# Optimization experiments

Hardware: AMD Instinct MI355X
Metric: run time of the kernel (lower is better)

Reference implementation:

```python
import jax, jax.numpy as jnp
import numpy as np

K_CHAINS, N_STATES, ALPHABET, SEQ_LEN = 3, 12, 32, 64


def setup_inputs() -> dict:
    key = jax.random.key(0)
    k0, k1, k2, k3, k4 = jax.random.split(key, 5)
    return {
        "ys": jax.random.randint(k0, (SEQ_LEN,), 0, ALPHABET),
        "transition": jax.random.normal(k1, (K_CHAINS, N_STATES, N_STATES), jnp.float32),
        "emission": jax.random.normal(k2, (K_CHAINS, N_STATES, ALPHABET), jnp.float32),
        "choice": jax.random.normal(k3, (K_CHAINS,), jnp.float32),
        "prior": jax.random.normal(k4, (K_CHAINS, N_STATES), jnp.float32),
    }


def reference(ys, transition, emission, choice, prior):
    K, S = transition.shape[0], transition.shape[1]
    c = jax.nn.log_softmax(choice)                  # (K,)
    t = jax.nn.log_softmax(transition, axis=-1)     # (K,S,S)
    e = jax.nn.log_softmax(emission, axis=-1)       # (K,S,A)
    p = jax.nn.log_softmax(prior, axis=-1)          # (K,S)

    # enumerate expanded state space: tuples (s_1..s_K, i) -> N = S^K * K rows
    grids = jnp.meshgrid(*([jnp.arange(S)] * K + [jnp.arange(K)]), indexing="ij")
    tbl = jnp.stack(grids, -1).reshape(-1, K + 1)   # (N, K+1)
    states = tbl[:, :K]                             # (N, K) chain states
    chain = tbl[:, K]                               # (N,)   active chain index

    # transition matrix A[m, n] = logprob(old expanded state n -> new expanded state m)
    onehot = jax.nn.one_hot(chain, K, dtype=bool)   # (N, K)
    eq = states[:, None, :] == states[None, :, :]   # (N_new, N_old, K)
    valid = jnp.where(onehot[:, None, :], True, eq).all(-1)  # non-active chains unchanged
    s_new = jnp.take_along_axis(states, chain[:, None], axis=1)[:, 0]  # (N,) new state of active chain
    s_old = states[:, chain]                        # (N_old, N_new): old state at chain[m]
    t_term = t[chain[None, :], s_old, s_new[None, :]]  # (N_old, N_new)
    Amat = c[chain][:, None] + t_term.T + jnp.where(valid, 0.0, -jnp.inf)  # (N_new, N_old)

    # emission table B[m, y] = e[chain[m], state of active chain, y]
    B = e[chain, s_new]                             # (N, A)

    # initial alpha: sum_j p[j, s_j] + c[i]
    alpha0 = p[jnp.arange(K)[None, :], states].sum(-1) + c[chain]  # (N,)

    def step(alpha, y):
        alpha = B[:, y] + jax.nn.logsumexp(alpha[None, :] + Amat, axis=-1)
        return alpha, None

    alpha, _ = jax.lax.scan(step, alpha0, ys)
    return jax.nn.logsumexp(alpha)
```

## Files before the change

kernel.cpp:

```cpp
#include <hip/hip_runtime.h>
#include <math.h>

#define KC 3
#define S 12
#define SS 1728
#define AB 32
#define TLEN 64
#define NTHREADS 448
#define NWAVES 7
#define NSLICE 432
#define ROWW 13
#define LN2F 0.69314718055994530942f

__global__ __launch_bounds__(NTHREADS, 2)
void hmm_fwd_kernel(const int* __restrict__ ys,
                    const float* __restrict__ transition,
                    const float* __restrict__ emission,
                    const float* __restrict__ choice,
                    const float* __restrict__ prior,
                    float* __restrict__ out)
{
    __shared__ float P0[144*ROWW], P1[144*ROWW], P2[144*ROWW];
    __shared__ float BR[144*ROWW], BQ[144*ROWW], BP[144*ROWW];
    __shared__ float ECt[KC*AB*S];
    __shared__ float T_s[KC][S][S];
    __shared__ float p_lin[KC][S];
    __shared__ float c_lin[KC];
    __shared__ int   ys_s[TLEN];
    __shared__ float wsum[NWAVES];

    const int tid = threadIdx.x;

    if (tid < TLEN) ys_s[tid] = ys[tid];

    if (tid == 0) {
        float m = fmaxf(fmaxf(choice[0], choice[1]), choice[2]);
        float e0 = __expf(choice[0]-m), e1 = __expf(choice[1]-m), e2 = __expf(choice[2]-m);
        float inv = 1.f / (e0+e1+e2);
        c_lin[0] = e0*inv; c_lin[1] = e1*inv; c_lin[2] = e2*inv;
    }
    if (tid >= 1 && tid < 1 + KC) {
        int k = tid - 1;
        float m = -INFINITY;
        #pragma unroll
        for (int i = 0; i < S; ++i) m = fmaxf(m, prior[k*S + i]);
        float ev[S]; float s = 0.f;
        #pragma unroll
        for (int i = 0; i < S; ++i) { ev[i] = __expf(prior[k*S + i] - m); s += ev[i]; }
        float inv = 1.f / s;
        #pragma unroll
        for (int i = 0; i < S; ++i) p_lin[k][i] = ev[i] * inv;
    }
    if (tid >= 64 && tid < 64 + KC*S) {
        int r = tid - 64;
        int k = r / S, i = r % S;
        const float* row = transition + (k*S + i)*S;
        float m = -INFINITY;
        #pragma unroll
        for (int j = 0; j < S; ++j) m = fmaxf(m, row[j]);
        float ev[S]; float s = 0.f;
        #pragma unroll
        for (int j = 0; j < S; ++j) { ev[j] = __expf(row[j] - m); s += ev[j]; }
        float inv = 1.f / s;
        #pragma unroll
        for (int j = 0; j < S; ++j) T_s[k][i][j] = ev[j] * inv;
    }
    if (tid >= 128 && tid < 128 + KC*S) {
        int r = tid - 128;
        int k = r / S, sj = r % S;
        float cm = fmaxf(fmaxf(choice[0], choice[1]), choice[2]);
        float ce = __expf(choice[k]-cm) /
                   (__expf(choice[0]-cm) + __expf(choice[1]-cm) + __expf(choice[2]-cm));
        const float* row = emission + (k*S + sj)*AB;
        float m = -INFINITY;
        #pragma unroll
        for (int a = 0; a < AB; ++a) m = fmaxf(m, row[a]);
        float ev[AB]; float s = 0.f;
        #pragma unroll
        for (int a = 0; a < AB; ++a) { ev[a] = __expf(row[a] - m); s += ev[a]; }
        float inv = ce / s;
        #pragma unroll
        for (int a = 0; a < AB; ++a) ECt[(k*AB + a)*S + sj] = ev[a] * inv;
    }
    __syncthreads();

    const bool active = tid < NSLICE;
    const int sk = tid / 144;
    const int q  = tid % 144;

    const float* rdp = (sk == 0) ? &BR[ROWW*q] : (sk == 1) ? &BQ[ROWW*q] : &BP[ROWW*q];
    float*       wrp = (sk == 0) ? &P0[ROWW*q] : (sk == 1) ? &P1[ROWW*q] : &P2[ROWW*q];
    const float* ecb = &ECt[sk*AB*S];

    const int s0f = tid / 36;
    const int s1f = (4*tid % 144) / 12;
    const int s2b = (4*tid) % 12;
    const int bRo = ROWW*(12*s1f + s2b) + s0f;
    const int bQo = ROWW*(12*s0f + s2b) + s1f;
    const int bPo = ROWW*(12*s0f + s1f) + s2b;

    float Treg[S][S];
    if (active) {
        #pragma unroll
        for (int i = 0; i < S; ++i) {
            #pragma unroll
            for (int j = 0; j < S; ++j) {
                float tmp = T_s[sk][i][j];
                asm volatile("v_mov_b32 %0, %1" : "=v"(Treg[i][j]) : "v"(tmp));
            }
        }
        float pq = (sk == 0) ? p_lin[1][q/12] * p_lin[2][q%12]
                 : (sk == 1) ? p_lin[0][q/12] * p_lin[2][q%12]
                 :             p_lin[0][q/12] * p_lin[1][q%12];
        float ck = c_lin[sk];
        #pragma unroll
        for (int j = 0; j < S; ++j) wrp[j] = p_lin[sk][j] * pq * ck;
    }
    __syncthreads();

    float logR = 0.f, invR = 1.f;

    for (int t = 0; t < TLEN; ++t) {
        const int y = ys_s[t];

        if (active) {
            float b[4];
            #pragma unroll
            for (int e = 0; e < 4; ++e) {
                float r = P0[bRo + ROWW*e];
                float g = P1[bQo + ROWW*e];
                float h = P2[bPo + e];
                b[e] = (r + g + h) * invR;
            }
            #pragma unroll
            for (int e = 0; e < 4; ++e) {
                BR[bRo + ROWW*e] = b[e];
                BQ[bQo + ROWW*e] = b[e];
                BP[bPo + e]      = b[e];
            }
        }
        __syncthreads();

        float o[S];
        if (active) {
            const float* eb = &ecb[y*S];
            float4 e0 = *reinterpret_cast<const float4*>(&eb[0]);
            float4 e1 = *reinterpret_cast<const float4*>(&eb[4]);
            float4 e2 = *reinterpret_cast<const float4*>(&eb[8]);

            float bv[S];
            #pragma unroll
            for (int i = 0; i < S; ++i) bv[i] = rdp[i];

            float acc[S];
            #pragma unroll
            for (int j = 0; j < S; ++j) acc[j] = 0.f;
            #pragma unroll
            for (int i = 0; i < S; ++i) {
                const float bb = bv[i];
                #pragma unroll
                for (int j = 0; j < S; ++j) acc[j] = __builtin_fmaf(bb, Treg[i][j], acc[j]);
            }
            o[0] = acc[0]*e0.x; o[1] = acc[1]*e0.y; o[2]  = acc[2]*e0.z;  o[3]  = acc[3]*e0.w;
            o[4] = acc[4]*e1.x; o[5] = acc[5]*e1.y; o[6]  = acc[6]*e1.z;  o[7]  = acc[7]*e1.w;
            o[8] = acc[8]*e2.x; o[9] = acc[9]*e2.y; o[10] = acc[10]*e2.z; o[11] = acc[11]*e2.w;

            #pragma unroll
            for (int j = 0; j < S; ++j) wrp[j] = o[j];
        }

        if ((t & 7) == 7) {
            float part = 0.f;
            if (active) {
                #pragma unroll
                for (int j = 0; j < S; ++j) part += o[j];
            }
            #pragma unroll
            for (int w = 32; w > 0; w >>= 1) part += __shfl_xor(part, w);
            if ((tid & 63) == 0) wsum[tid >> 6] = part;
        }
        __syncthreads();

        if ((t & 7) == 7 && t < TLEN-1) {
            float R = wsum[0];
            #pragma unroll
            for (int w = 1; w < NWAVES; ++w) R += wsum[w];
            invR = __builtin_amdgcn_rcpf(R);
            logR += __log2f(R);
        } else {
            invR = 1.f;
        }
    }

    if (tid == 0) {
        float R = wsum[0];
        #pragma unroll
        for (int w = 1; w < NWAVES; ++w) R += wsum[w];
        out[0] = LN2F * (__log2f(R) + logR);
    }
}

extern "C" void kernel_launch(void* const* d_in, const int* in_sizes, int n_in,
                              void* d_out, int out_size, void* d_ws, size_t ws_size,
                              hipStream_t stream) {
    const int*   ys         = (const int*)  d_in[0];
    const float* transition = (const float*)d_in[1];
    const float* emission   = (const float*)d_in[2];
    const float* choice     = (const float*)d_in[3];
    const float* prior      = (const float*)d_in[4];
    float* out = (float*)d_out;

    hipLaunchKernelGGL(hmm_fwd_kernel, dim3(1), dim3(NTHREADS), 0, stream,
                       ys, transition, emission, choice, prior, out);
}
```

Baseline: 71.25 us.

## Fuse gather-sum into step with double-buffered planes, one barrier per step

Drops the separate gather/scatter phase (BR/BQ/BP buffers) and its extra barrier. Each thread now reads the two foreign-chain planes directly with strided LDS loads and keeps its own slice in registers. The per-step output is double-buffered so only one __syncthreads is needed per time step. Transition rows are no longer pinned in registers but read from LDS as float4 broadcasts each step, which trades register pressure for extra LDS traffic.

```diff
diff --git a/kernel.cpp b/kernel.cpp
--- a/kernel.cpp
+++ b/kernel.cpp
@@ -9,7 +9,6 @@
 #define NTHREADS 448
 #define NWAVES 7
 #define NSLICE 432
-#define ROWW 13
 #define LN2F 0.69314718055994530942f
 
 __global__ __launch_bounds__(NTHREADS, 2)
@@ -20,10 +19,9 @@
                     const float* __restrict__ prior,
                     float* __restrict__ out)
 {
-    __shared__ float P0[144*ROWW], P1[144*ROWW], P2[144*ROWW];
-    __shared__ float BR[144*ROWW], BQ[144*ROWW], BP[144*ROWW];
-    __shared__ float ECt[KC*AB*S];
-    __shared__ float T_s[KC][S][S];
+    __shared__ __align__(16) float PL[2][KC][SS];
+    __shared__ __align__(16) float T_s[KC][S][S];
+    __shared__ __align__(16) float ECt[KC][AB][S];
     __shared__ float p_lin[KC][S];
     __shared__ float c_lin[KC];
     __shared__ int   ys_s[TLEN];
@@ -80,100 +78,112 @@
         for (int a = 0; a < AB; ++a) { ev[a] = __expf(row[a] - m); s += ev[a]; }
         float inv = ce / s;
         #pragma unroll
-        for (int a = 0; a < AB; ++a) ECt[(k*AB + a)*S + sj] = ev[a] * inv;
+        for (int a = 0; a < AB; ++a) ECt[k][a][sj] = ev[a] * inv;
     }
     __syncthreads();
 
     const bool active = tid < NSLICE;
-    const int sk = tid / 144;
-    const int q  = tid % 144;
-
-    const float* rdp = (sk == 0) ? &BR[ROWW*q] : (sk == 1) ? &BQ[ROWW*q] : &BP[ROWW*q];
-    float*       wrp = (sk == 0) ? &P0[ROWW*q] : (sk == 1) ? &P1[ROWW*q] : &P2[ROWW*q];
-    const float* ecb = &ECt[sk*AB*S];
-
-    const int s0f = tid / 36;
-    const int s1f = (4*tid % 144) / 12;
-    const int s2b = (4*tid) % 12;
-    const int bRo = ROWW*(12*s1f + s2b) + s0f;
-    const int bQo = ROWW*(12*s0f + s2b) + s1f;
-    const int bPo = ROWW*(12*s0f + s1f) + s2b;
-
-    float Treg[S][S];
+    const int ct = active ? tid : (NSLICE - 1);
+    const int sk = ct / 144;
+    const int q  = ct % 144;
+    const int qh = q / 12, ql = q % 12;
+
+    int offA, offB;
+    if (sk == 0)      { offA = 12*ql + qh;        offB = 12*qh + ql;        }
+    else if (sk == 1) { offA = 12*ql + qh;        offB = 144*qh + ql;       }
+    else              { offA = 144*ql + qh;       offB = 144*qh + ql;       }
+
+    const int fApl = (sk == 0) ? 1 : 0;
+    const int fBpl = (sk == 2) ? 1 : 2;
+
+    const float* Tp  = &T_s[sk][0][0];
+    const float* ecp = &ECt[sk][0][0];
+
+    const float* fA0 = &PL[0][fApl][offA];
+    const float* fB0 = &PL[0][fBpl][offB];
+    float*       wp0 = &PL[0][sk][12*q];
+    const float* fA1 = &PL[1][fApl][offA];
+    const float* fB1 = &PL[1][fBpl][offB];
+    float*       wp1 = &PL[1][sk][12*q];
+
+    float own[S];
     if (active) {
-        #pragma unroll
-        for (int i = 0; i < S; ++i) {
-            #pragma unroll
-            for (int j = 0; j < S; ++j) {
-                float tmp = T_s[sk][i][j];
-                asm volatile("v_mov_b32 %0, %1" : "=v"(Treg[i][j]) : "v"(tmp));
-            }
-        }
-        float pq = (sk == 0) ? p_lin[1][q/12] * p_lin[2][q%12]
-                 : (sk == 1) ? p_lin[0][q/12] * p_lin[2][q%12]
-                 :             p_lin[0][q/12] * p_lin[1][q%12];
+        float pq = (sk == 0) ? p_lin[1][qh] * p_lin[2][ql]
+                 : (sk == 1) ? p_lin[0][qh] * p_lin[2][ql]
+                 :             p_lin[0][qh] * p_lin[1][ql];
         float ck = c_lin[sk];
         #pragma unroll
-        for (int j = 0; j < S; ++j) wrp[j] = p_lin[sk][j] * pq * ck;
+        for (int j = 0; j < S; ++j) {
+            own[j] = p_lin[sk][j] * pq * ck;
+            wp0[j] = own[j];
+        }
     }
     __syncthreads();
 
     float logR = 0.f, invR = 1.f;
 
-    for (int t = 0; t < TLEN; ++t) {
+    auto do_step = [&](int t, const float* fA, const float* fB, float* wp) {
         const int y = ys_s[t];
-
         if (active) {
-            float b[4];
-            #pragma unroll
-            for (int e = 0; e < 4; ++e) {
-                float r = P0[bRo + ROWW*e];
-                float g = P1[bQo + ROWW*e];
-                float h = P2[bPo + e];
-                b[e] = (r + g + h) * invR;
-            }
-            #pragma unroll
-            for (int e = 0; e < 4; ++e) {
-                BR[bRo + ROWW*e] = b[e];
-                BQ[bQo + ROWW*e] = b[e];
-                BP[bPo + e]      = b[e];
-            }
-        }
-        __syncthreads();
-
-        float o[S];
-        if (active) {
-            const float* eb = &ecb[y*S];
+            const float* eb = ecp + y*S;
             float4 e0 = *reinterpret_cast<const float4*>(&eb[0]);
             float4 e1 = *reinterpret_cast<const float4*>(&eb[4]);
             float4 e2 = *reinterpret_cast<const float4*>(&eb[8]);
 
+            float fa[S], fb[S];
+            if (sk == 0) {
+                #pragma unroll
+                for (int i = 0; i < S; ++i) { fa[i] = fA[144*i]; fb[i] = fB[144*i]; }
+            } else if (sk == 1) {
+                #pragma unroll
+                for (int i = 0; i < S; ++i) { fa[i] = fA[144*i]; fb[i] = fB[12*i]; }
+            } else {
+                #pragma unroll
+                for (int i = 0; i < S; ++i) { fa[i] = fA[12*i];  fb[i] = fB[12*i]; }
+            }
+
             float bv[S];
             #pragma unroll
-            for (int i = 0; i < S; ++i) bv[i] = rdp[i];
+            for (int i = 0; i < S; ++i) bv[i] = (own[i] + fa[i] + fb[i]) * invR;
 
             float acc[S];
             #pragma unroll
             for (int j = 0; j < S; ++j) acc[j] = 0.f;
             #pragma unroll
             for (int i = 0; i < S; ++i) {
+                float4 t0 = *reinterpret_cast<const float4*>(&Tp[12*i + 0]);
+                float4 t1 = *reinterpret_cast<const float4*>(&Tp[12*i + 4]);
+                float4 t2 = *reinterpret_cast<const float4*>(&Tp[12*i + 8]);
                 const float bb = bv[i];
-                #pragma unroll
-                for (int j = 0; j < S; ++j) acc[j] = __builtin_fmaf(bb, Treg[i][j], acc[j]);
+                acc[0] = __builtin_fmaf(bb, t0.x, acc[0]);
+                acc[1] = __builtin_fmaf(bb, t0.y, acc[1]);
+                acc[2] = __builtin_fmaf(bb, t0.z, acc[2]);
+                acc[3] = __builtin_fmaf(bb, t0.w, acc[3]);
+                acc[4] = __builtin_fmaf(bb, t1.x, acc[4]);
+                acc[5] = __builtin_fmaf(bb, t1.y, acc[5]);
+                acc[6] = __builtin_fmaf(bb, t1.z, acc[6]);
+                acc[7] = __builtin_fmaf(bb, t1.w, acc[7]);
+                acc[8] = __builtin_fmaf(bb, t2.x, acc[8]);
+                acc[9] = __builtin_fmaf(bb, t2.y, acc[9]);
+                acc[10] = __builtin_fmaf(bb, t2.z, acc[10]);
+                acc[11] = __builtin_fmaf(bb, t2.w, acc[11]);
             }
-            o[0] = acc[0]*e0.x; o[1] = acc[1]*e0.y; o[2]  = acc[2]*e0.z;  o[3]  = acc[3]*e0.w;
-            o[4] = acc[4]*e1.x; o[5] = acc[5]*e1.y; o[6]  = acc[6]*e1.z;  o[7]  = acc[7]*e1.w;
-            o[8] = acc[8]*e2.x; o[9] = acc[9]*e2.y; o[10] = acc[10]*e2.z; o[11] = acc[11]*e2.w;
-
-            #pragma unroll
-            for (int j = 0; j < S; ++j) wrp[j] = o[j];
+
+            own[0]=acc[0]*e0.x; own[1]=acc[1]*e0.y; own[2] =acc[2]*e0.z;  own[3] =acc[3]*e0.w;
+            own[4]=acc[4]*e1.x; own[5]=acc[5]*e1.y; own[6] =acc[6]*e1.z;  own[7] =acc[7]*e1.w;
+            own[8]=acc[8]*e2.x; own[9]=acc[9]*e2.y; own[10]=acc[10]*e2.z; own[11]=acc[11]*e2.w;
+
+            float4* pw = reinterpret_cast<float4*>(wp);
+            pw[0] = make_float4(own[0], own[1], own[2],  own[3]);
+            pw[1] = make_float4(own[4], own[5], own[6],  own[7]);
+            pw[2] = make_float4(own[8], own[9], own[10], own[11]);
         }
 
         if ((t & 7) == 7) {
             float part = 0.f;
             if (active) {
                 #pragma unroll
-                for (int j = 0; j < S; ++j) part += o[j];
+                for (int j = 0; j < S; ++j) part += own[j];
             }
             #pragma unroll
             for (int w = 32; w > 0; w >>= 1) part += __shfl_xor(part, w);
@@ -190,6 +200,11 @@
         } else {
             invR = 1.f;
         }
+    };
+
+    for (int tt = 0; tt < TLEN; tt += 2) {
+        do_step(tt,     fA0, fB0, wp1);
+        do_step(tt + 1, fA1, fB1, wp0);
     }
 
     if (tid == 0) {
```

Result: slower. 96.61 us (+35.6%).

## Split each transition slice across two threads with unified alpha layout

Applied to the files above, without the earlier changes.

Doubles the thread count so each thread computes 6 of the 12 output states of a chain slice, halving per-thread FMA work and register-resident transition data. Replaces the three padded, permuted P/B buffers with per-chain APL arrays in natural state order plus a single BETA array, using strided or vector reads per chain. The intent is to shorten the serial per-timestep critical path on a single-block launch. The cost is more waves taking part in every barrier and strided shared-memory accesses that may cause bank conflicts.

```diff
diff --git a/kernel.cpp b/kernel.cpp
--- a/kernel.cpp
+++ b/kernel.cpp
@@ -6,13 +6,12 @@
 #define SS 1728
 #define AB 32
 #define TLEN 64
-#define NTHREADS 448
-#define NWAVES 7
-#define NSLICE 432
-#define ROWW 13
+#define NTHREADS 896
+#define NWAVES 14
+#define NACT 864
 #define LN2F 0.69314718055994530942f
 
-__global__ __launch_bounds__(NTHREADS, 2)
+__global__ __launch_bounds__(NTHREADS, 4)
 void hmm_fwd_kernel(const int* __restrict__ ys,
                     const float* __restrict__ transition,
                     const float* __restrict__ emission,
@@ -20,9 +19,9 @@
                     const float* __restrict__ prior,
                     float* __restrict__ out)
 {
-    __shared__ float P0[144*ROWW], P1[144*ROWW], P2[144*ROWW];
-    __shared__ float BR[144*ROWW], BQ[144*ROWW], BP[144*ROWW];
-    __shared__ float ECt[KC*AB*S];
+    __shared__ __align__(16) float APL[KC][SS];
+    __shared__ __align__(16) float BETA[SS];
+    __shared__ __align__(16) float ECt[KC][AB][16];
     __shared__ float T_s[KC][S][S];
     __shared__ float p_lin[KC][S];
     __shared__ float c_lin[KC];
@@ -79,112 +78,127 @@
         #pragma unroll
         for (int a = 0; a < AB; ++a) { ev[a] = __expf(row[a] - m); s += ev[a]; }
         float inv = ce / s;
-        #pragma unroll
-        for (int a = 0; a < AB; ++a) ECt[(k*AB + a)*S + sj] = ev[a] * inv;
+        const int slot = (sj / 6) * 8 + (sj % 6);
+        #pragma unroll
+        for (int a = 0; a < AB; ++a) ECt[k][a][slot] = ev[a] * inv;
     }
     __syncthreads();
 
-    const bool active = tid < NSLICE;
-    const int sk = tid / 144;
-    const int q  = tid % 144;
-
-    const float* rdp = (sk == 0) ? &BR[ROWW*q] : (sk == 1) ? &BQ[ROWW*q] : &BP[ROWW*q];
-    float*       wrp = (sk == 0) ? &P0[ROWW*q] : (sk == 1) ? &P1[ROWW*q] : &P2[ROWW*q];
-    const float* ecb = &ECt[sk*AB*S];
-
-    const int s0f = tid / 36;
-    const int s1f = (4*tid % 144) / 12;
-    const int s2b = (4*tid) % 12;
-    const int bRo = ROWW*(12*s1f + s2b) + s0f;
-    const int bQo = ROWW*(12*s0f + s2b) + s1f;
-    const int bPo = ROWW*(12*s0f + s1f) + s2b;
-
-    float Treg[S][S];
-    if (active) {
+    const bool act = tid < NACT;
+    const int ct = act ? tid : (NACT - 1);
+    const int sl = ct >> 1;
+    const int h  = ct & 1;
+    const int sk = sl / 144;
+    const int q  = sl % 144;
+    const int qh = q / 12, ql = q % 12;
+
+    const int rdb = (sk == 0) ? q : (sk == 1) ? 144*qh + ql : 12*q;
+    const int wstr = (sk == 0) ? 144 : (sk == 1) ? 12 : 1;
+    const int wbas = rdb + wstr * 6 * h;
+    float* const wap = &APL[sk][wbas];
+    const float* const ecp = &ECt[sk][0][8*h];
+
+    float Trg[S][6];
+    if (act) {
         #pragma unroll
         for (int i = 0; i < S; ++i) {
             #pragma unroll
-            for (int j = 0; j < S; ++j) {
-                float tmp = T_s[sk][i][j];
-                asm volatile("v_mov_b32 %0, %1" : "=v"(Treg[i][j]) : "v"(tmp));
-            }
-        }
-        float pq = (sk == 0) ? p_lin[1][q/12] * p_lin[2][q%12]
-                 : (sk == 1) ? p_lin[0][q/12] * p_lin[2][q%12]
-                 :             p_lin[0][q/12] * p_lin[1][q%12];
-        float ck = c_lin[sk];
-        #pragma unroll
-        for (int j = 0; j < S; ++j) wrp[j] = p_lin[sk][j] * pq * ck;
+            for (int m = 0; m < 6; ++m) Trg[i][m] = T_s[sk][i][6*h + m];
+        }
+    }
+
+    if (act) {
+        const int sA = 2*tid;
+        const int a0 = sA/144, b0 = (sA/12)%12, c0 = sA%12;
+        const float pp = p_lin[0][a0]*p_lin[1][b0];
+        const float pA = pp*p_lin[2][c0], pB = pp*p_lin[2][c0+1];
+        #pragma unroll
+        for (int k = 0; k < KC; ++k) {
+            float2 v; v.x = pA*c_lin[k]; v.y = pB*c_lin[k];
+            *reinterpret_cast<float2*>(&APL[k][sA]) = v;
+        }
     }
     __syncthreads();
 
     float logR = 0.f, invR = 1.f;
-
+    const int s2p = 2*tid;
+
+    #pragma unroll 1
     for (int t = 0; t < TLEN; ++t) {
         const int y = ys_s[t];
 
-        if (active) {
-            float b[4];
-            #pragma unroll
-            for (int e = 0; e < 4; ++e) {
-                float r = P0[bRo + ROWW*e];
-                float g = P1[bQo + ROWW*e];
-                float h = P2[bPo + e];
-                b[e] = (r + g + h) * invR;
+        if (act) {
+            float2 a0 = *reinterpret_cast<const float2*>(&APL[0][s2p]);
+            float2 a1 = *reinterpret_cast<const float2*>(&APL[1][s2p]);
+            float2 a2 = *reinterpret_cast<const float2*>(&APL[2][s2p]);
+            float2 b;
+            b.x = (a0.x + a1.x + a2.x) * invR;
+            b.y = (a0.y + a1.y + a2.y) * invR;
+            *reinterpret_cast<float2*>(&BETA[s2p]) = b;
+        }
+        __syncthreads();
+
+        float acc0=0.f, acc1=0.f, acc2=0.f, acc3=0.f, acc4=0.f, acc5=0.f;
+        if (act) {
+            float4 e03 = *reinterpret_cast<const float4*>(&ecp[y*16]);
+            float2 e45 = *reinterpret_cast<const float2*>(&ecp[y*16 + 4]);
+
+            float bv[S];
+            if (sk == 0) {
+                #pragma unroll
+                for (int i = 0; i < S; ++i) bv[i] = BETA[rdb + 144*i];
+            } else if (sk == 1) {
+                #pragma unroll
+                for (int i = 0; i < S; ++i) bv[i] = BETA[rdb + 12*i];
+            } else {
+                float4 r0 = *reinterpret_cast<const float4*>(&BETA[rdb + 0]);
+                float4 r1 = *reinterpret_cast<const float4*>(&BETA[rdb + 4]);
+                float4 r2 = *reinterpret_cast<const float4*>(&BETA[rdb + 8]);
+                bv[0]=r0.x; bv[1]=r0.y; bv[2] =r0.z; bv[3] =r0.w;
+                bv[4]=r1.x; bv[5]=r1.y; bv[6] =r1.z; bv[7] =r1.w;
+                bv[8]=r2.x; bv[9]=r2.y; bv[10]=r2.z; bv[11]=r2.w;
             }
-            #pragma unroll
-            for (int e = 0; e < 4; ++e) {
-                BR[bRo + ROWW*e] = b[e];
-                BQ[bQo + ROWW*e] = b[e];
-                BP[bPo + e]      = b[e];
-            }
-        }
-        __syncthreads();
-
-        float o[S];
-        if (active) {
-            const float* eb = &ecb[y*S];
-            float4 e0 = *reinterpret_cast<const float4*>(&eb[0]);
-            float4 e1 = *reinterpret_cast<const float4*>(&eb[4]);
-            float4 e2 = *reinterpret_cast<const float4*>(&eb[8]);
-
-            float bv[S];
-            #pragma unroll
-            for (int i = 0; i < S; ++i) bv[i] = rdp[i];
-
-            float acc[S];
-            #pragma unroll
-            for (int j = 0; j < S; ++j) acc[j] = 0.f;
+
             #pragma unroll
             for (int i = 0; i < S; ++i) {
                 const float bb = bv[i];
-                #pragma unroll
-                for (int j = 0; j < S; ++j) acc[j] = __builtin_fmaf(bb, Treg[i][j], acc[j]);
+                acc0 = __builtin_fmaf(bb, Trg[i][0], acc0);
+                acc1 = __builtin_fmaf(bb, Trg[i][1], acc1);
+                acc2 = __builtin_fmaf(bb, Trg[i][2], acc2);
+                acc3 = __builtin_fmaf(bb, Trg[i][3], acc3);
+                acc4 = __builtin_fmaf(bb, Trg[i][4], acc4);
+                acc5 = __builtin_fmaf(bb, Trg[i][5], acc5);
             }
-            o[0] = acc[0]*e0.x; o[1] = acc[1]*e0.y; o[2]  = acc[2]*e0.z;  o[3]  = acc[3]*e0.w;
-            o[4] = acc[4]*e1.x; o[5] = acc[5]*e1.y; o[6]  = acc[6]*e1.z;  o[7]  = acc[7]*e1.w;
-            o[8] = acc[8]*e2.x; o[9] = acc[9]*e2.y; o[10] = acc[10]*e2.z; o[11] = acc[11]*e2.w;
-
+            acc0 *= e03.x; acc1 *= e03.y; acc2 *= e03.z;
+            acc3 *= e03.w; acc4 *= e45.x; acc5 *= e45.y;
+
+            if (sk == 2) {
+                if (h == 0) {
+                    *reinterpret_cast<float4*>(&wap[0]) = make_float4(acc0, acc1, acc2, acc3);
+                    *reinterpret_cast<float2*>(&wap[4]) = make_float2(acc4, acc5);
+                } else {
+                    *reinterpret_cast<float2*>(&wap[0]) = make_float2(acc0, acc1);
+                    *reinterpret_cast<float4*>(&wap[2]) = make_float4(acc2, acc3, acc4, acc5);
+                }
+            } else {
+                wap[0*wstr] = acc0; wap[1*wstr] = acc1; wap[2*wstr] = acc2;
+                wap[3*wstr] = acc3; wap[4*wstr] = acc4; wap[5*wstr] = acc5;
+            }
+        }
+
+        if ((t & 7) == 7) {
+            float part = acc0 + acc1 + acc2 + acc3 + acc4 + acc5;
+            part += __shfl_xor(part, 32); part += __shfl_xor(part, 16);
+            part += __shfl_xor(part, 8);  part += __shfl_xor(part, 4);
+            part += __shfl_xor(part, 2);  part += __shfl_xor(part, 1);
+            if ((tid & 63) == 0) wsum[tid >> 6] = part;
+        }
+        __syncthreads();
+
+        if ((t & 7) == 7 && t < TLEN-1) {
+            float R = 0.f;
             #pragma unroll
-            for (int j = 0; j < S; ++j) wrp[j] = o[j];
-        }
-
-        if ((t & 7) == 7) {
-            float part = 0.f;
-            if (active) {
-                #pragma unroll
-                for (int j = 0; j < S; ++j) part += o[j];
-            }
-            #pragma unroll
-            for (int w = 32; w > 0; w >>= 1) part += __shfl_xor(part, w);
-            if ((tid & 63) == 0) wsum[tid >> 6] = part;
-        }
-        __syncthreads();
-
-        if ((t & 7) == 7 && t < TLEN-1) {
-            float R = wsum[0];
-            #pragma unroll
-            for (int w = 1; w < NWAVES; ++w) R += wsum[w];
+            for (int w = 0; w < NWAVES; ++w) R += wsum[w];
             invR = __builtin_amdgcn_rcpf(R);
             logR += __log2f(R);
         } else {
@@ -193,9 +207,9 @@
     }
 
     if (tid == 0) {
-        float R = wsum[0];
-        #pragma unroll
-        for (int w = 1; w < NWAVES; ++w) R += wsum[w];
+        float R = 0.f;
+        #pragma unroll
+        for (int w = 0; w < NWAVES; ++w) R += wsum[w];
         out[0] = LN2F * (__log2f(R) + logR);
     }
 }
```

After: 60.34 us. -15.3%, faster.
